# Kernel optimization log

Measured on AMD Instinct MI355X. Metric: run time of the kernel, lower is better.

## Reference

```python
import jax, jax.numpy as jnp
import numpy as np
import math

T, B, V, D = 8, 32, 50257, 256
N = 4096            # memory slots
H = 4               # attention heads
L = 2               # transformer layers
K = 3               # shift width
HALF = K // 2
WIN = 16            # controller window
RH, WH = 1, 1       # read / write heads
EPS = 1e-12


def _pe(win, d):
    pos = jnp.arange(win, dtype=jnp.float32)[:, None]
    div = jnp.exp(jnp.arange(0, d, 2, dtype=jnp.float32) * (-math.log(10000.0) / d))
    pe = jnp.zeros((win, d), dtype=jnp.float32)
    pe = pe.at[:, 0::2].set(jnp.sin(pos * div))
    pe = pe.at[:, 1::2].set(jnp.cos(pos * div))
    return pe[:, None, :]


def _ln(x, g, b, eps=1e-5):
    mu = x.mean(-1, keepdims=True)
    var = ((x - mu) ** 2).mean(-1, keepdims=True)
    return (x - mu) * jax.lax.rsqrt(var + eps) * g + b


def _mha(x, Wqkv, bqkv, Wo, bo):
    S, Bc, Dm = x.shape
    dh = Dm // H
    qkv = x @ Wqkv.T + bqkv
    q, k, v = jnp.split(qkv, 3, axis=-1)
    q = q.reshape(S, Bc, H, dh)
    k = k.reshape(S, Bc, H, dh)
    v = v.reshape(S, Bc, H, dh)
    logits = jnp.einsum('sbhd,tbhd->bhst', q, k) / math.sqrt(dh)
    a = jax.nn.softmax(logits, axis=-1)
    o = jnp.einsum('bhst,tbhd->sbhd', a, v).reshape(S, Bc, Dm)
    return o @ Wo.T + bo


def _addressing(key_v, beta, gate, shift, gamma, prev_w, memory):
    # key_v [B,M], beta/gate/gamma [B,1], shift [B,K], prev_w [B,N], memory [B,N,M]
    key_n = key_v / (jnp.linalg.norm(key_v, axis=-1, keepdims=True) + EPS)
    mem_n = memory / (jnp.linalg.norm(memory, axis=-1, keepdims=True) + EPS)
    cos = jnp.einsum('bnm,bm->bn', mem_n, key_n)
    wc = jax.nn.softmax(jax.nn.softplus(beta) * cos, axis=-1)
    g = jax.nn.sigmoid(gate)
    wg = g * wc + (1.0 - g) * prev_w
    s = jax.nn.softmax(shift, axis=-1)
    shifted = sum(s[:, k:k + 1] * jnp.roll(wg, k - HALF, axis=-1) for k in range(K))
    gp = 1.0 + jax.nn.softplus(gamma)
    wt = (shifted + EPS) ** gp
    return wt / (wt.sum(-1, keepdims=True) + EPS)


def setup_inputs() -> dict:
    key = jax.random.key(0)
    ks = iter(jax.random.split(key, 40))
    def w(shape, s=0.02):
        return jax.random.normal(next(ks), shape, jnp.float32) * s
    return {
        'tokens': jax.random.randint(next(ks), (T, B), 0, V, jnp.int32),
        'emb_W': w((V, D)),
        'read_gate_W': w((D, D)), 'read_gate_b': jnp.zeros((D,)),
        'film_W': w((2 * D, D)), 'film_b': jnp.zeros((2 * D,)),
        't_Wqkv': w((L, 3 * D, D)), 't_bqkv': jnp.zeros((L, 3 * D)),
        't_Wo': w((L, D, D)), 't_bo': jnp.zeros((L, D)),
        't_ln1_g': jnp.ones((L, D)), 't_ln1_b': jnp.zeros((L, D)),
        't_ln2_g': jnp.ones((L, D)), 't_ln2_b': jnp.zeros((L, D)),
        't_W1': w((L, 4 * D, D)), 't_b1': jnp.zeros((L, 4 * D)),
        't_W2': w((L, D, 4 * D)), 't_b2': jnp.zeros((L, D)),
        'out_ln_g': jnp.ones((D,)), 'out_ln_b': jnp.zeros((D,)),
        'lstm_Wih': w((2, 4 * D, D)), 'lstm_Whh': w((2, 4 * D, D)),
        'lstm_bih': jnp.zeros((2, 4 * D)), 'lstm_bhh': jnp.zeros((2, 4 * D)),
        'head_W': w((V, D)), 'head_b': jnp.zeros((V,)),
        'read_W': w((D + 3 + K, D)), 'read_b': jnp.zeros((D + 3 + K,)),
        'write_W': w((3 * D + 3 + K, D)), 'write_b': jnp.zeros((3 * D + 3 + K,)),
    }


def reference(tokens, emb_W, read_gate_W, read_gate_b, film_W, film_b,
              t_Wqkv, t_bqkv, t_Wo, t_bo, t_ln1_g, t_ln1_b, t_ln2_g, t_ln2_b,
              t_W1, t_b1, t_W2, t_b2, out_ln_g, out_ln_b,
              lstm_Wih, lstm_Whh, lstm_bih, lstm_bhh,
              head_W, head_b, read_W, read_b, write_W, write_b):
    pe = _pe(WIN, D)
    memory = jnp.zeros((B, N, D), jnp.float32)
    read_w = jnp.zeros((B, RH, N), jnp.float32).at[:, :, 0].set(1.0)
    write_w = jnp.zeros((B, WH, N), jnp.float32).at[:, :, 0].set(1.0)
    record = jnp.zeros((B, D), jnp.float32)
    hx = jnp.zeros((2, B, D), jnp.float32)
    cx = jnp.zeros((2, B, D), jnp.float32)
    hist = jnp.zeros((1, B, D), jnp.float32)
    logits_all = []
    for t in range(T):  # T fixed, sequential recurrence (context length grows)
        emb = emb_W[tokens[t]]                               # [B,D]
        r = jnp.einsum('bhn,bnm->bm', read_w, memory)        # sum over read heads
        fp = record @ film_W.T + film_b
        gam = 1.0 + jnp.tanh(fp[:, :D])
        bet = fp[:, D:]
        rg = jax.nn.sigmoid(record @ read_gate_W.T + read_gate_b)
        x_in = gam * emb + bet + rg * r
        ctx = jnp.concatenate([hist, x_in[None]], axis=0)
        if ctx.shape[0] > WIN:
            ctx = ctx[-WIN:]
        hist = ctx
        h = ctx + pe[:ctx.shape[0]]
        for l in range(L):  # norm_first pre-LN encoder layers (eval, relu FFN)
            h = h + _mha(_ln(h, t_ln1_g[l], t_ln1_b[l]), t_Wqkv[l], t_bqkv[l], t_Wo[l], t_bo[l])
            h = h + (jax.nn.relu(_ln(h, t_ln2_g[l], t_ln2_b[l]) @ t_W1[l].T + t_b1[l]) @ t_W2[l].T + t_b2[l])
        c_out = _ln(h[-1], out_ln_g, out_ln_b)
        # 2-layer LSTM single step (torch gate order i,f,g,o)
        x_l = c_out
        new_h, new_c = [], []
        for l in range(2):
            gates = x_l @ lstm_Wih[l].T + lstm_bih[l] + hx[l] @ lstm_Whh[l].T + lstm_bhh[l]
            i_g, f_g, g_g, o_g = jnp.split(gates, 4, axis=-1)
            c_new = jax.nn.sigmoid(f_g) * cx[l] + jax.nn.sigmoid(i_g) * jnp.tanh(g_g)
            h_new = jax.nn.sigmoid(o_g) * jnp.tanh(c_new)
            new_h.append(h_new); new_c.append(c_new)
            x_l = h_new
        hx = jnp.stack(new_h); cx = jnp.stack(new_c)
        record = hx[-1]
        c_out = c_out + x_l
        logits_all.append(c_out @ head_W.T + head_b)
        # read addressing
        rp = (c_out @ read_W.T + read_b).reshape(B, RH, -1)
        new_rw = []
        for hh in range(RH):
            p = rp[:, hh]
            new_rw.append(_addressing(p[:, :D], p[:, D:D + 1], p[:, D + 1:D + 2],
                                      p[:, D + 2:D + 2 + K], p[:, D + 2 + K:D + 3 + K],
                                      read_w[:, hh], memory))
        read_w = jnp.stack(new_rw, axis=1)
        # write addressing + erase/add (addressing uses pre-update memory)
        wp = (c_out @ write_W.T + write_b).reshape(B, WH, -1)
        mem_pre = memory
        new_ww = []
        for hh in range(WH):
            p = wp[:, hh]
            wt = _addressing(p[:, :D], p[:, D:D + 1], p[:, D + 1:D + 2],
                             p[:, D + 2:D + 2 + K], p[:, D + 2 + K:D + 3 + K],
                             write_w[:, hh], mem_pre)
            erase = jax.nn.sigmoid(p[:, D + 3 + K:2 * D + 3 + K])
            add = jnp.tanh(p[:, 2 * D + 3 + K:3 * D + 3 + K])
            memory = memory * (1.0 - wt[:, :, None] * erase[:, None, :]) + wt[:, :, None] * add[:, None, :]
            new_ww.append(wt)
        write_w = jnp.stack(new_ww, axis=1)
    return jnp.stack(logits_all, axis=0)  # [T, B, V]
```

## Files before the change

### kernel.cpp

```cpp
#include <hip/hip_runtime.h>
#include <math.h>

#define TT 8
#define BB 32
#define VV 50257
#define DD 256
#define NN 4096
#define EPS_ 1e-12f

typedef __attribute__((ext_vector_type(8))) short short8;
typedef __attribute__((ext_vector_type(4))) float f32x4;

__device__ __forceinline__ float sigf(float x) { return 1.f / (1.f + expf(-x)); }
__device__ __forceinline__ float softplusf_(float x) { return fmaxf(x, 0.f) + log1pf(expf(-fabsf(x))); }
__device__ __forceinline__ unsigned f2bf(float f) {
  union { float f; unsigned u; } c; c.f = f;
  return (c.u + 0x7FFFu + ((c.u >> 16) & 1u)) >> 16;
}
__device__ __forceinline__ float bf2f(unsigned u16) {
  union { unsigned u; float f; } c; c.u = u16 << 16; return c.f;
}

__device__ __forceinline__ float blk_sum(float v, float* s) {
#pragma unroll
  for (int o = 32; o > 0; o >>= 1) v += __shfl_down(v, o);
  __syncthreads();
  if ((threadIdx.x & 63) == 0) s[threadIdx.x >> 6] = v;
  __syncthreads();
  return s[0] + s[1] + s[2] + s[3];
}
__device__ __forceinline__ float blk_max(float v, float* s) {
#pragma unroll
  for (int o = 32; o > 0; o >>= 1) v = fmaxf(v, __shfl_down(v, o));
  __syncthreads();
  if ((threadIdx.x & 63) == 0) s[threadIdx.x >> 6] = v;
  __syncthreads();
  return fmaxf(fmaxf(s[0], s[1]), fmaxf(s[2], s[3]));
}

__global__ void init_k(float* rw, float* ww, float* hpe) {
  int i = blockIdx.x * 256 + threadIdx.x;
  if (i < BB) { rw[(size_t)i * NN] = 1.f; ww[(size_t)i * NN] = 1.f; }
  if (i < BB * DD) hpe[i] = (i & 1) ? 1.f : 0.f;
}

__global__ void cvtw_k(const float* __restrict__ W, unsigned short* __restrict__ Wh, int n4) {
  int i = blockIdx.x * 256 + threadIdx.x;
  if (i >= n4) return;
  float4 v = *(const float4*)(W + (size_t)i * 4);
  uint2 p;
  p.x = f2bf(v.x) | (f2bf(v.y) << 16);
  p.y = f2bf(v.z) | (f2bf(v.w) << 16);
  *(uint2*)(Wh + (size_t)i * 4) = p;
}

__global__ void catlstm_k(const float* __restrict__ Wih, const float* __restrict__ Whh,
                          const float* __restrict__ bih, const float* __restrict__ bhh,
                          unsigned short* __restrict__ Wc, float* __restrict__ cb) {
  int i = blockIdx.x * 256 + threadIdx.x;
  if (i >= 2 * 1024 * 512) return;
  int k = i & 511, np = (i >> 9) & 1023, l = i >> 19;
  int d = np >> 2, gate = np & 3;
  int src = gate * 256 + d;
  float v = (k < 256) ? Wih[((size_t)l * 1024 + src) * 256 + k]
                      : Whh[((size_t)l * 1024 + src) * 256 + (k - 256)];
  Wc[i] = (unsigned short)f2bf(v);
  if (k == 0) cb[l * 1024 + np] = bih[l * 1024 + src] + bhh[l * 1024 + src];
}

__global__ void catrw_k(const float* __restrict__ rW, const float* __restrict__ rb,
                        const float* __restrict__ wW, const float* __restrict__ wb,
                        unsigned short* __restrict__ Wrw, float* __restrict__ brw) {
  int i = blockIdx.x * 256 + threadIdx.x;
  if (i >= 1036 * 256) return;
  int k = i & 255, n = i >> 8;
  float v = (n < 262) ? rW[(size_t)n * 256 + k] : wW[(size_t)(n - 262) * 256 + k];
  Wrw[i] = (unsigned short)f2bf(v);
  if (k == 0) brw[n] = (n < 262) ? rb[n] : wb[n - 262];
}

__global__ void brc_k(const float* __restrict__ fb, const float* __restrict__ rb, float* __restrict__ brc) {
  int i = blockIdx.x * 256 + threadIdx.x;
  if (i < 512) brc[i] = fb[i];
  else if (i < 768) brc[i] = rb[i - 512];
}

__global__ __launch_bounds__(256) void ln0_k(const float* __restrict__ hpe,
                                             const float* __restrict__ g1, const float* __restrict__ b1,
                                             unsigned short* __restrict__ q1b) {
  __shared__ float s8[8];
  int b = blockIdx.x, d = threadIdx.x;
  float v = hpe[(size_t)b * 256 + d];
  float mu = blk_sum(v, s8) * (1.f / 256.f);
  float dd = v - mu;
  float var = blk_sum(dd * dd, s8) * (1.f / 256.f);
  float rs = rsqrtf(var + 1e-5f);
  q1b[(size_t)b * 256 + d] = (unsigned short)f2bf(dd * rs * g1[d] + b1[d]);
}

template <int EPI>
__global__ __launch_bounds__(256) void gA_k(const unsigned short* __restrict__ A,
                                            const unsigned short* __restrict__ W,
                                            const float* __restrict__ bias,
                                            float* __restrict__ Cf,
                                            unsigned short* __restrict__ Cb,
                                            int ldc, int Nlim) {
  const int tid = threadIdx.x, w = tid >> 6, l = tid & 63, r = l & 15, q = l >> 4;
  const int m0 = blockIdx.y * 32;
  const int n = blockIdx.x * 64 + w * 16 + r;
  const unsigned short* Ap = A + (size_t)m0 * 256;
  const unsigned short* Wp = W + (size_t)n * 256;
  f32x4 acc0 = {0.f, 0.f, 0.f, 0.f}, acc1 = {0.f, 0.f, 0.f, 0.f};
#pragma unroll
  for (int kt = 0; kt < 8; ++kt) {
    short8 a0 = *(const short8*)(Ap + r * 256 + kt * 32 + q * 8);
    short8 a1 = *(const short8*)(Ap + (16 + r) * 256 + kt * 32 + q * 8);
    short8 bf = *(const short8*)(Wp + kt * 32 + q * 8);
    acc0 = __builtin_amdgcn_mfma_f32_16x16x32_bf16(a0, bf, acc0, 0, 0, 0);
    acc1 = __builtin_amdgcn_mfma_f32_16x16x32_bf16(a1, bf, acc1, 0, 0, 0);
  }
  if (n >= Nlim) return;
  float bb = bias[n];
#pragma unroll
  for (int e = 0; e < 4; ++e) {
    int m1 = m0 + q * 4 + e, m2 = m1 + 16;
    float v1 = acc0[e] + bb, v2 = acc1[e] + bb;
    if constexpr (EPI == 0) {
      Cf[(size_t)m1 * ldc + n] = v1;
      Cf[(size_t)m2 * ldc + n] = v2;
    } else {
      Cb[(size_t)m1 * ldc + n] = (unsigned short)f2bf(fmaxf(v1, 0.f));
      Cb[(size_t)m2 * ldc + n] = (unsigned short)f2bf(fmaxf(v2, 0.f));
    }
  }
}

template <int K, int OLN>
__global__ __launch_bounds__(256) void gB_k(const unsigned short* __restrict__ A,
                                            const unsigned short* __restrict__ W,
                                            const float* __restrict__ bias,
                                            const float* __restrict__ resid,
                                            float* __restrict__ Hout,
                                            const float* __restrict__ lng,
                                            const float* __restrict__ lnb,
                                            unsigned short* __restrict__ Xb, int xstride,
                                            float* __restrict__ c_out) {
  __shared__ float hv[32][260];
  const int tid = threadIdx.x, w = tid >> 6, l = tid & 63, r = l & 15, q = l >> 4;
  const int m0 = blockIdx.x * 32;
  const unsigned short* Ap = A + (size_t)m0 * K;
  const unsigned short* Wp0 = W + (size_t)(w * 64 + 0 + r) * K;
  const unsigned short* Wp1 = W + (size_t)(w * 64 + 16 + r) * K;
  const unsigned short* Wp2 = W + (size_t)(w * 64 + 32 + r) * K;
  const unsigned short* Wp3 = W + (size_t)(w * 64 + 48 + r) * K;
  f32x4 acc0[4], acc1[4];
#pragma unroll
  for (int j = 0; j < 4; ++j) { acc0[j] = {0.f, 0.f, 0.f, 0.f}; acc1[j] = {0.f, 0.f, 0.f, 0.f}; }
#pragma unroll 4
  for (int kt = 0; kt < K / 32; ++kt) {
    short8 a0 = *(const short8*)(Ap + (size_t)r * K + kt * 32 + q * 8);
    short8 a1 = *(const short8*)(Ap + (size_t)(16 + r) * K + kt * 32 + q * 8);
    short8 b0 = *(const short8*)(Wp0 + kt * 32 + q * 8);
    short8 b1 = *(const short8*)(Wp1 + kt * 32 + q * 8);
    short8 b2 = *(const short8*)(Wp2 + kt * 32 + q * 8);
    short8 b3 = *(const short8*)(Wp3 + kt * 32 + q * 8);
    acc0[0] = __builtin_amdgcn_mfma_f32_16x16x32_bf16(a0, b0, acc0[0], 0, 0, 0);
    acc1[0] = __builtin_amdgcn_mfma_f32_16x16x32_bf16(a1, b0, acc1[0], 0, 0, 0);
    acc0[1] = __builtin_amdgcn_mfma_f32_16x16x32_bf16(a0, b1, acc0[1], 0, 0, 0);
    acc1[1] = __builtin_amdgcn_mfma_f32_16x16x32_bf16(a1, b1, acc1[1], 0, 0, 0);
    acc0[2] = __builtin_amdgcn_mfma_f32_16x16x32_bf16(a0, b2, acc0[2], 0, 0, 0);
    acc1[2] = __builtin_amdgcn_mfma_f32_16x16x32_bf16(a1, b2, acc1[2], 0, 0, 0);
    acc0[3] = __builtin_amdgcn_mfma_f32_16x16x32_bf16(a0, b3, acc0[3], 0, 0, 0);
    acc1[3] = __builtin_amdgcn_mfma_f32_16x16x32_bf16(a1, b3, acc1[3], 0, 0, 0);
  }
#pragma unroll
  for (int j = 0; j < 4; ++j) {
    int n = w * 64 + j * 16 + r;
    float bb = bias[n];
#pragma unroll
    for (int e = 0; e < 4; ++e) {
      int m1 = q * 4 + e, m2 = m1 + 16;
      float v1 = acc0[j][e] + bb + resid[(size_t)(m0 + m1) * 256 + n];
      float v2 = acc1[j][e] + bb + resid[(size_t)(m0 + m2) * 256 + n];
      Hout[(size_t)(m0 + m1) * 256 + n] = v1;
      Hout[(size_t)(m0 + m2) * 256 + n] = v2;
      hv[m1][n] = v1;
      hv[m2][n] = v2;
    }
  }
  __syncthreads();
  const float4 g4 = *(const float4*)(lng + l * 4);
  const float4 be4 = *(const float4*)(lnb + l * 4);
#pragma unroll
  for (int i = 0; i < 8; ++i) {
    int row = w * 8 + i;
    float4 v = *(const float4*)&hv[row][l * 4];
    float s1 = v.x + v.y + v.z + v.w;
    float s2 = v.x * v.x + v.y * v.y + v.z * v.z + v.w * v.w;
#pragma unroll
    for (int o = 32; o > 0; o >>= 1) { s1 += __shfl_xor(s1, o); s2 += __shfl_xor(s2, o); }
    float mu = s1 * (1.f / 256.f);
    float var = fmaxf(s2 * (1.f / 256.f) - mu * mu, 0.f);
    float rs = rsqrtf(var + 1e-5f);
    float y0 = (v.x - mu) * rs * g4.x + be4.x;
    float y1 = (v.y - mu) * rs * g4.y + be4.y;
    float y2 = (v.z - mu) * rs * g4.z + be4.z;
    float y3 = (v.w - mu) * rs * g4.w + be4.w;
    uint2 pk;
    pk.x = f2bf(y0) | (f2bf(y1) << 16);
    pk.y = f2bf(y2) | (f2bf(y3) << 16);
    *(uint2*)(Xb + (size_t)(m0 + row) * xstride + l * 4) = pk;
    if constexpr (OLN) {
      float4 cv = make_float4(y0, y1, y2, y3);
      *(float4*)(c_out + (size_t)(m0 + row) * 256 + l * 4) = cv;
    }
  }
}

template <int LAST>
__global__ __launch_bounds__(256) void gL_k(const unsigned short* __restrict__ A,
                                            const unsigned short* __restrict__ W,
                                            const float* __restrict__ cbias,
                                            float* __restrict__ cx,
                                            unsigned short* __restrict__ li_own,
                                            unsigned short* __restrict__ li_next,
                                            const float* __restrict__ c_outp,
                                            unsigned short* __restrict__ cfinb,
                                            unsigned short* __restrict__ record_b) {
  __shared__ float g[32][68];
  const int tid = threadIdx.x, w = tid >> 6, l = tid & 63, r = l & 15, q = l >> 4;
  const int n = blockIdx.x * 64 + w * 16 + r;
  const unsigned short* Wp = W + (size_t)n * 512;
  f32x4 acc0 = {0.f, 0.f, 0.f, 0.f}, acc1 = {0.f, 0.f, 0.f, 0.f};
#pragma unroll 4
  for (int kt = 0; kt < 16; ++kt) {
    short8 a0 = *(const short8*)(A + (size_t)r * 512 + kt * 32 + q * 8);
    short8 a1 = *(const short8*)(A + (size_t)(16 + r) * 512 + kt * 32 + q * 8);
    short8 bf = *(const short8*)(Wp + kt * 32 + q * 8);
    acc0 = __builtin_amdgcn_mfma_f32_16x16x32_bf16(a0, bf, acc0, 0, 0, 0);
    acc1 = __builtin_amdgcn_mfma_f32_16x16x32_bf16(a1, bf, acc1, 0, 0, 0);
  }
  float bb = cbias[n];
  int nb = w * 16 + r;
#pragma unroll
  for (int e = 0; e < 4; ++e) {
    g[q * 4 + e][nb] = acc0[e] + bb;
    g[16 + q * 4 + e][nb] = acc1[e] + bb;
  }
  __syncthreads();
#pragma unroll
  for (int h2 = 0; h2 < 2; ++h2) {
    int u = tid + 256 * h2;
    int b = u >> 4, dd = u & 15;
    int dg = blockIdx.x * 16 + dd;
    float gi = g[b][dd * 4 + 0], gf = g[b][dd * 4 + 1];
    float gg = g[b][dd * 4 + 2], go = g[b][dd * 4 + 3];
    float c = sigf(gf) * cx[b * 256 + dg] + sigf(gi) * tanhf(gg);
    float hN = sigf(go) * tanhf(c);
    cx[b * 256 + dg] = c;
    li_own[(size_t)b * 512 + 256 + dg] = (unsigned short)f2bf(hN);
    if constexpr (LAST) {
      record_b[b * 256 + dg] = (unsigned short)f2bf(hN);
      cfinb[b * 256 + dg] = (unsigned short)f2bf(c_outp[b * 256 + dg] + hN);
    } else {
      li_next[(size_t)b * 512 + dg] = (unsigned short)f2bf(hN);
    }
  }
}

__global__ __launch_bounds__(256) void xinpw_k(const int* __restrict__ tokens,
                                               const float* __restrict__ embW,
                                               const float* __restrict__ fp,
                                               const float* __restrict__ rvec,
                                               const float* __restrict__ g1, const float* __restrict__ b1,
                                               float* __restrict__ hpe,
                                               unsigned short* __restrict__ q1b, int t) {
  __shared__ float s8[8];
  int b = blockIdx.x, d = threadIdx.x;
  float gam = 1.f + tanhf(fp[(size_t)b * 768 + d]);
  float bet = fp[(size_t)b * 768 + 256 + d];
  float rg = sigf(fp[(size_t)b * 768 + 512 + d]);
  int tok = tokens[t * BB + b];
  float emb = embW[(size_t)tok * 256 + d];
  float ang = (float)(t + 1) * expf(-logf(10000.f) * (float)(d & ~1) / 256.f);
  float pe = (d & 1) ? cosf(ang) : sinf(ang);
  float x = gam * emb + bet + rg * rvec[b * 256 + d] + pe;
  hpe[((size_t)(t + 1) * BB + b) * 256 + d] = x;
  float mu = blk_sum(x, s8) * (1.f / 256.f);
  float dd = x - mu;
  float var = blk_sum(dd * dd, s8) * (1.f / 256.f);
  float rs = rsqrtf(var + 1e-5f);
  q1b[((size_t)(t + 1) * BB + b) * 256 + d] = (unsigned short)f2bf(dd * rs * g1[d] + b1[d]);
}

__global__ __launch_bounds__(128) void attn_k(const float* __restrict__ qkv,
                                              unsigned short* __restrict__ ao, int S) {
  int bh = blockIdx.x;
  int b = bh >> 2, h = bh & 3;
  __shared__ float q[9][64], k[9][64], v[9][64], lg[9][12];
  int tid = threadIdx.x;
  for (int i = tid; i < S * 64; i += 128) {
    int s = i >> 6, d = i & 63;
    const float* base = qkv + (size_t)(s * BB + b) * 768 + h * 64 + d;
    q[s][d] = base[0]; k[s][d] = base[256]; v[s][d] = base[512];
  }
  __syncthreads();
  for (int p = tid; p < S * S; p += 128) {
    int s = p / S, t2 = p % S;
    float acc = 0.f;
    for (int d = 0; d < 64; ++d) acc += q[s][d] * k[t2][d];
    lg[s][t2] = acc * 0.125f;
  }
  __syncthreads();
  if (tid < S) {
    float mx = -1e30f;
    for (int t2 = 0; t2 < S; ++t2) mx = fmaxf(mx, lg[tid][t2]);
    float sum = 0.f;
    for (int t2 = 0; t2 < S; ++t2) { float e = expf(lg[tid][t2] - mx); lg[tid][t2] = e; sum += e; }
    float inv = 1.f / sum;
    for (int t2 = 0; t2 < S; ++t2) lg[tid][t2] *= inv;
  }
  __syncthreads();
  for (int i = tid; i < S * 64; i += 128) {
    int s = i >> 6, d = i & 63;
    float o = 0.f;
    for (int t2 = 0; t2 < S; ++t2) o += lg[s][t2] * v[t2][d];
    ao[(size_t)(s * BB + b) * 256 + h * 64 + d] = (unsigned short)f2bf(o);
  }
}

__global__ __launch_bounds__(64) void attnl_k(const float* __restrict__ qkv,
                                              unsigned short* __restrict__ ao, int S) {
  int bh = blockIdx.x;
  int b = bh >> 2, h = bh & 3;
  int d = threadIdx.x;
  __shared__ float sc[9];
  float qd = qkv[(size_t)((S - 1) * BB + b) * 768 + h * 64 + d];
  for (int j = 0; j < S; ++j) {
    float p = qd * qkv[(size_t)(j * BB + b) * 768 + h * 64 + 256 + d];
#pragma unroll
    for (int o = 32; o > 0; o >>= 1) p += __shfl_down(p, o);
    if (d == 0) sc[j] = p * 0.125f;
  }
  __syncthreads();
  float mx = -1e30f;
  for (int j = 0; j < S; ++j) mx = fmaxf(mx, sc[j]);
  float pj[9], sum = 0.f;
  for (int j = 0; j < S; ++j) { pj[j] = expf(sc[j] - mx); sum += pj[j]; }
  float inv = 1.f / sum;
  float o = 0.f;
  for (int j = 0; j < S; ++j) o += pj[j] * inv * qkv[(size_t)(j * BB + b) * 768 + h * 64 + 512 + d];
  ao[(size_t)b * 256 + h * 64 + d] = (unsigned short)f2bf(o);
}

__global__ __launch_bounds__(256) void head_k(const unsigned short* __restrict__ Wh,
                                              const unsigned short* __restrict__ Ah,
                                              const float* __restrict__ hb,
                                              float* __restrict__ out) {
  const int tid = threadIdx.x;
  const int w = tid >> 6, l = tid & 63;
  const int r = l & 15, q = l >> 4;
  const int n = blockIdx.x * 64 + w * 16 + r;
  const int nc = n < VV ? n : VV - 1;
  const short* Ap = (const short*)Ah;
  const short* Wp = (const short*)Wh + (size_t)nc * 256;
  short8 a0[8], a1[8], bf[8];
#pragma unroll
  for (int kt = 0; kt < 8; ++kt) {
    a0[kt] = *(const short8*)(Ap + r * 256 + kt * 32 + q * 8);
    a1[kt] = *(const short8*)(Ap + (16 + r) * 256 + kt * 32 + q * 8);
    bf[kt] = *(const short8*)(Wp + kt * 32 + q * 8);
  }
  f32x4 acc0 = {0.f, 0.f, 0.f, 0.f}, acc1 = {0.f, 0.f, 0.f, 0.f};
#pragma unroll
  for (int kt = 0; kt < 8; ++kt) {
    acc0 = __builtin_amdgcn_mfma_f32_16x16x32_bf16(a0[kt], bf[kt], acc0, 0, 0, 0);
    acc1 = __builtin_amdgcn_mfma_f32_16x16x32_bf16(a1[kt], bf[kt], acc1, 0, 0, 0);
  }
  if (n < VV) {
    float bb = hb[n];
#pragma unroll
    for (int e = 0; e < 4; ++e) {
      int m = q * 4 + e;
      out[(size_t)m * VV + n] = acc0[e] + bb;
      out[(size_t)(16 + m) * VV + n] = acc1[e] + bb;
    }
  }
}

__global__ __launch_bounds__(256) void passA_k(const unsigned short* __restrict__ mem,
                                               const float* __restrict__ rpwp,
                                               float* __restrict__ dr,
                                               float* __restrict__ dw,
                                               float* __restrict__ nrm) {
  __shared__ float kr[256], kw[256];
  int b = blockIdx.y, tid = threadIdx.x;
  kr[tid] = rpwp[(size_t)b * 1036 + tid];
  kw[tid] = rpwp[(size_t)b * 1036 + 262 + tid];
  __syncthreads();
  int w = tid >> 6, lane = tid & 63;
  float4 kr4 = *(float4*)&kr[lane * 4];
  float4 kw4 = *(float4*)&kw[lane * 4];
  int n0 = blockIdx.x * 16 + w * 4;
  for (int rr = 0; rr < 4; ++rr) {
    int n = n0 + rr;
    const unsigned short* row = mem + ((size_t)b * NN + n) * 256;
    uint2 p = *(const uint2*)(row + lane * 4);
    float m0 = bf2f(p.x & 0xffffu), m1 = bf2f(p.x >> 16);
    float m2 = bf2f(p.y & 0xffffu), m3 = bf2f(p.y >> 16);
    float pr = m0 * kr4.x + m1 * kr4.y + m2 * kr4.z + m3 * kr4.w;
    float pw = m0 * kw4.x + m1 * kw4.y + m2 * kw4.z + m3 * kw4.w;
    float pn = m0 * m0 + m1 * m1 + m2 * m2 + m3 * m3;
#pragma unroll
    for (int o = 32; o > 0; o >>= 1) {
      pr += __shfl_down(pr, o); pw += __shfl_down(pw, o); pn += __shfl_down(pn, o);
    }
    if (lane == 0) {
      dr[(size_t)b * NN + n] = pr;
      dw[(size_t)b * NN + n] = pw;
      nrm[(size_t)b * NN + n] = pn;
    }
  }
}

__global__ __launch_bounds__(256) void addr_k(const float* __restrict__ dr,
                                              const float* __restrict__ dw,
                                              const float* __restrict__ nrm,
                                              const float* __restrict__ rpwp,
                                              float* rw, float* ww,
                                              float* __restrict__ ea,
                                              float* __restrict__ rvec) {
  __shared__ float wg[4096];
  __shared__ float s8[8];
  int head = blockIdx.x & 1, b = blockIdx.x >> 1;
  int tid = threadIdx.x;
  const float* p = rpwp + (size_t)b * 1036 + (head ? 262 : 0);
  const float* dot = (head ? dw : dr) + (size_t)b * NN;
  const float* n2 = nrm + (size_t)b * NN;
  float* wout = (head ? ww : rw) + (size_t)b * NN;

  float kv = p[tid];
  float kn = sqrtf(blk_sum(kv * kv, s8)) + EPS_;
  float beta = p[256], gate = p[257], sh0 = p[258], sh1 = p[259], sh2 = p[260], gamma = p[261];
  float spb = softplusf_(beta);
  float g = sigf(gate);
  float mx3 = fmaxf(sh0, fmaxf(sh1, sh2));
  float e0 = expf(sh0 - mx3), e1 = expf(sh1 - mx3), e2 = expf(sh2 - mx3);
  float esum = e0 + e1 + e2;
  float s0 = e0 / esum, s1 = e1 / esum, s2 = e2 / esum;
  float gp = 1.f + softplusf_(gamma);

  float l[16];
  float lmax = -1e30f;
#pragma unroll
  for (int i = 0; i < 16; ++i) {
    int n = tid + i * 256;
    float cs = dot[n] / ((sqrtf(n2[n]) + EPS_) * kn);
    l[i] = spb * cs;
    lmax = fmaxf(lmax, l[i]);
  }
  float Mx = blk_max(lmax, s8);
  float es = 0.f;
#pragma unroll
  for (int i = 0; i < 16; ++i) { l[i] = expf(l[i] - Mx); es += l[i]; }
  float SS = blk_sum(es, s8);
  float inv = 1.f / SS;
#pragma unroll
  for (int i = 0; i < 16; ++i) {
    int n = tid + i * 256;
    wg[n] = g * l[i] * inv + (1.f - g) * wout[n];
  }
  __syncthreads();
  float wt[16];
  float wsum = 0.f;
#pragma unroll
  for (int i = 0; i < 16; ++i) {
    int n = tid + i * 256;
    float sh = s0 * wg[(n + 1) & 4095] + s1 * wg[n] + s2 * wg[(n + 4095) & 4095];
    wt[i] = powf(sh + EPS_, gp);
    wsum += wt[i];
  }
  float WS = blk_sum(wsum, s8) + EPS_;
  float winv = 1.f / WS;
#pragma unroll
  for (int i = 0; i < 16; ++i) wout[tid + i * 256] = wt[i] * winv;

  if (head) {
    ea[(size_t)b * 512 + tid] = sigf(p[262 + tid]);
    ea[(size_t)b * 512 + 256 + tid] = tanhf(p[518 + tid]);
  } else {
    rvec[(size_t)b * 256 + tid] = 0.f;
  }
}

template <int FIRST>
__global__ __launch_bounds__(256) void passB_k(unsigned short* mem, const float* __restrict__ ww,
                                               const float* __restrict__ rw,
                                               const float* __restrict__ ea,
                                               float* __restrict__ rvec) {
  __shared__ float eS[256], aS[256];
  __shared__ float rred[4][256];
  int b = blockIdx.y, tid = threadIdx.x;
  eS[tid] = ea[(size_t)b * 512 + tid];
  aS[tid] = ea[(size_t)b * 512 + 256 + tid];
  __syncthreads();
  int w = tid >> 6, lane = tid & 63;
  float4 e4 = *(float4*)&eS[lane * 4];
  float4 a4 = *(float4*)&aS[lane * 4];
  float4 racc = make_float4(0.f, 0.f, 0.f, 0.f);
  int n0 = blockIdx.x * 128 + w * 32;
  for (int rr = 0; rr < 32; ++rr) {
    int n = n0 + rr;
    float wt = ww[(size_t)b * NN + n];
    float rwv = rw[(size_t)b * NN + n];
    unsigned short* row = mem + ((size_t)b * NN + n) * 256;
    float m0, m1, m2, m3;
    if (FIRST) {
      m0 = wt * a4.x; m1 = wt * a4.y; m2 = wt * a4.z; m3 = wt * a4.w;
    } else {
      uint2 p = *(const uint2*)(row + lane * 4);
      m0 = bf2f(p.x & 0xffffu) * (1.f - wt * e4.x) + wt * a4.x;
      m1 = bf2f(p.x >> 16) * (1.f - wt * e4.y) + wt * a4.y;
      m2 = bf2f(p.y & 0xffffu) * (1.f - wt * e4.z) + wt * a4.z;
      m3 = bf2f(p.y >> 16) * (1.f - wt * e4.w) + wt * a4.w;
    }
    uint2 pk;
    pk.x = f2bf(m0) | (f2bf(m1) << 16);
    pk.y = f2bf(m2) | (f2bf(m3) << 16);
    *(uint2*)(row + lane * 4) = pk;
    racc.x += rwv * m0; racc.y += rwv * m1; racc.z += rwv * m2; racc.w += rwv * m3;
  }
  rred[w][lane * 4 + 0] = racc.x;
  rred[w][lane * 4 + 1] = racc.y;
  rred[w][lane * 4 + 2] = racc.z;
  rred[w][lane * 4 + 3] = racc.w;
  __syncthreads();
  float s = rred[0][tid] + rred[1][tid] + rred[2][tid] + rred[3][tid];
  atomicAdd(rvec + (size_t)b * 256 + tid, s);
}

extern "C" void kernel_launch(void* const* d_in, const int* in_sizes, int n_in,
                              void* d_out, int out_size, void* d_ws, size_t ws_size,
                              hipStream_t stream) {
  const int* tokens = (const int*)d_in[0];
  const float* emb_W = (const float*)d_in[1];
  const float* read_gate_W = (const float*)d_in[2];
  const float* read_gate_b = (const float*)d_in[3];
  const float* film_W = (const float*)d_in[4];
  const float* film_b = (const float*)d_in[5];
  const float* t_Wqkv = (const float*)d_in[6];
  const float* t_bqkv = (const float*)d_in[7];
  const float* t_Wo = (const float*)d_in[8];
  const float* t_bo = (const float*)d_in[9];
  const float* t_ln1_g = (const float*)d_in[10];
  const float* t_ln1_b = (const float*)d_in[11];
  const float* t_ln2_g = (const float*)d_in[12];
  const float* t_ln2_b = (const float*)d_in[13];
  const float* t_W1 = (const float*)d_in[14];
  const float* t_b1 = (const float*)d_in[15];
  const float* t_W2 = (const float*)d_in[16];
  const float* t_b2 = (const float*)d_in[17];
  const float* out_ln_g = (const float*)d_in[18];
  const float* out_ln_b = (const float*)d_in[19];
  const float* lstm_Wih = (const float*)d_in[20];
  const float* lstm_Whh = (const float*)d_in[21];
  const float* lstm_bih = (const float*)d_in[22];
  const float* lstm_bhh = (const float*)d_in[23];
  const float* head_W = (const float*)d_in[24];
  const float* head_b = (const float*)d_in[25];
  const float* read_W = (const float*)d_in[26];
  const float* read_b = (const float*)d_in[27];
  const float* write_W = (const float*)d_in[28];
  const float* write_b = (const float*)d_in[29];
  float* out = (float*)d_out;

  float* ws = (float*)d_ws;
  size_t off = 0;
  float* read_w = ws + off; off += (size_t)BB * NN;
  float* write_w = ws + off; off += (size_t)BB * NN;
  float* cx = ws + off; off += 2 * BB * DD;
  float* r_vec = ws + off; off += BB * DD;
  float* dot_r = ws + off; off += (size_t)BB * NN;
  float* dot_w = ws + off; off += (size_t)BB * NN;
  float* norm2 = ws + off; off += (size_t)BB * NN;
  unsigned short* record_b = (unsigned short*)(ws + off); off += BB * DD / 2;
  unsigned short* lstm_in_b = (unsigned short*)(ws + off); off += 2 * BB * 512 / 2;
  size_t zero_floats = off;
  unsigned short* memory = (unsigned short*)(ws + off); off += (size_t)BB * NN * DD / 2;
  float* hpe = ws + off; off += 9 * BB * DD;
  float* h = ws + off; off += 9 * BB * DD;
  float* h2 = ws + off; off += BB * DD;
  float* qkvC = ws + off; off += 9 * BB * 768;
  float* qkv2 = ws + off; off += 9 * BB * 768;
  float* fp = ws + off; off += BB * 768;
  float* c_out = ws + off; off += BB * DD;
  float* rpwp = ws + off; off += BB * 1036;
  float* ea = ws + off; off += BB * 2 * DD;
  unsigned short* q1b = (unsigned short*)(ws + off); off += 9 * BB * DD / 2;
  unsigned short* q2b = (unsigned short*)(ws + off); off += 9 * BB * DD / 2;
  unsigned short* x2b = (unsigned short*)(ws + off); off += 9 * BB * DD / 2;
  unsigned short* x2b2 = (unsigned short*)(ws + off); off += BB * DD / 2;
  unsigned short* ao_b = (unsigned short*)(ws + off); off += 9 * BB * DD / 2;
  unsigned short* ao2_b = (unsigned short*)(ws + off); off += BB * DD / 2;
  unsigned short* mid_b = (unsigned short*)(ws + off); off += 9 * BB * 1024 / 2;
  unsigned short* cfinb = (unsigned short*)(ws + off); off += BB * DD / 2;
  unsigned short* Wh = (unsigned short*)(ws + off); off += (size_t)VV * 256 / 2;
  unsigned short* Wq_b = (unsigned short*)(ws + off); off += 2 * 768 * 256 / 2;
  unsigned short* Wo_b = (unsigned short*)(ws + off); off += 2 * 256 * 256 / 2;
  unsigned short* W1_b = (unsigned short*)(ws + off); off += 2 * 1024 * 256 / 2;
  unsigned short* W2_b = (unsigned short*)(ws + off); off += 2 * 256 * 1024 / 2;
  unsigned short* Wc_b = (unsigned short*)(ws + off); off += 2 * 1024 * 512 / 2;
  unsigned short* Wrw_b = (unsigned short*)(ws + off); off += 1088 * 256 / 2;
  unsigned short* FR_b = (unsigned short*)(ws + off); off += 768 * 256 / 2;
  float* cb2 = ws + off; off += 2 * 1024;
  float* brw = ws + off; off += 1040;
  float* brc = ws + off; off += 768;
  if (ws_size < off * sizeof(float)) return;

  (void)hipMemsetAsync(ws, 0, zero_floats * sizeof(float), stream);
  (void)hipMemsetAsync(Wrw_b + (size_t)1036 * 256, 0, (size_t)52 * 256 * 2, stream);
  init_k<<<32, 256, 0, stream>>>(read_w, write_w, hpe);
  cvtw_k<<<(VV * 256 / 4 + 255) / 256, 256, 0, stream>>>(head_W, Wh, VV * 256 / 4);
  cvtw_k<<<(2 * 768 * 256 / 4 + 255) / 256, 256, 0, stream>>>(t_Wqkv, Wq_b, 2 * 768 * 256 / 4);
  cvtw_k<<<(2 * 256 * 256 / 4 + 255) / 256, 256, 0, stream>>>(t_Wo, Wo_b, 2 * 256 * 256 / 4);
  cvtw_k<<<(2 * 1024 * 256 / 4 + 255) / 256, 256, 0, stream>>>(t_W1, W1_b, 2 * 1024 * 256 / 4);
  cvtw_k<<<(2 * 256 * 1024 / 4 + 255) / 256, 256, 0, stream>>>(t_W2, W2_b, 2 * 256 * 1024 / 4);
  cvtw_k<<<(512 * 256 / 4 + 255) / 256, 256, 0, stream>>>(film_W, FR_b, 512 * 256 / 4);
  cvtw_k<<<(256 * 256 / 4 + 255) / 256, 256, 0, stream>>>(read_gate_W, FR_b + 512 * 256, 256 * 256 / 4);
  catlstm_k<<<4096, 256, 0, stream>>>(lstm_Wih, lstm_Whh, lstm_bih, lstm_bhh, Wc_b, cb2);
  catrw_k<<<1036, 256, 0, stream>>>(read_W, read_b, write_W, write_b, Wrw_b, brw);
  brc_k<<<3, 256, 0, stream>>>(film_b, read_gate_b, brc);
  ln0_k<<<BB, 256, 0, stream>>>(hpe, t_ln1_g, t_ln1_b, q1b);
  gA_k<0><<<dim3(12, 1), 256, 0, stream>>>(q1b, Wq_b, t_bqkv, qkvC, nullptr, 768, 768);

  for (int t = 0; t < TT; ++t) {
    const int S = t + 2;

    gA_k<0><<<dim3(12, 1), 256, 0, stream>>>(record_b, FR_b, brc, fp, nullptr, 768, 768);
    xinpw_k<<<BB, 256, 0, stream>>>(tokens, emb_W, fp, r_vec, t_ln1_g, t_ln1_b, hpe, q1b, t);
    gA_k<0><<<dim3(12, 1), 256, 0, stream>>>(q1b + (size_t)(t + 1) * BB * 256, Wq_b, t_bqkv,
                                             qkvC + (size_t)(t + 1) * BB * 768, nullptr, 768, 768);
    attn_k<<<BB * 4, 128, 0, stream>>>(qkvC, ao_b, S);
    gB_k<256, 0><<<S, 256, 0, stream>>>(ao_b, Wo_b, t_bo, hpe, h, t_ln2_g, t_ln2_b, x2b, 256, nullptr);
    gA_k<1><<<dim3(16, S), 256, 0, stream>>>(x2b, W1_b, t_b1, nullptr, mid_b, 1024, 1024);
    gB_k<1024, 0><<<S, 256, 0, stream>>>(mid_b, W2_b, t_b2, h, h, t_ln1_g + 256, t_ln1_b + 256, q2b, 256, nullptr);

    gA_k<0><<<dim3(12, S), 256, 0, stream>>>(q2b, Wq_b + 768 * 256, t_bqkv + 768, qkv2, nullptr, 768, 768);
    attnl_k<<<BB * 4, 64, 0, stream>>>(qkv2, ao2_b, S);
    gB_k<256, 0><<<1, 256, 0, stream>>>(ao2_b, Wo_b + 256 * 256, t_bo + 256, h + (size_t)(S - 1) * BB * 256,
                                        h2, t_ln2_g + 256, t_ln2_b + 256, x2b2, 256, nullptr);
    gA_k<1><<<dim3(16, 1), 256, 0, stream>>>(x2b2, W1_b + 1024 * 256, t_b1 + 1024, nullptr, mid_b, 1024, 1024);
    gB_k<1024, 1><<<1, 256, 0, stream>>>(mid_b, W2_b + 256 * 1024, t_b2 + 256, h2, h2,
                                         out_ln_g, out_ln_b, lstm_in_b, 512, c_out);

    gL_k<0><<<16, 256, 0, stream>>>(lstm_in_b, Wc_b, cb2, cx, lstm_in_b, lstm_in_b + BB * 512,
                                    nullptr, nullptr, nullptr);
    gL_k<1><<<16, 256, 0, stream>>>(lstm_in_b + BB * 512, Wc_b + (size_t)1024 * 512, cb2 + 1024,
                                    cx + BB * DD, lstm_in_b + BB * 512, nullptr, c_out, cfinb, record_b);

    head_k<<<(VV + 63) / 64, 256, 0, stream>>>(Wh, cfinb, head_b, out + (size_t)t * BB * VV);

    if (t < TT - 1) {
      gA_k<0><<<dim3(17, 1), 256, 0, stream>>>(cfinb, Wrw_b, brw, rpwp, nullptr, 1036, 1036);
      if (t > 0)
        passA_k<<<dim3(NN / 16, BB), 256, 0, stream>>>(memory, rpwp, dot_r, dot_w, norm2);
      addr_k<<<2 * BB, 256, 0, stream>>>(dot_r, dot_w, norm2, rpwp, read_w, write_w, ea, r_vec);
      if (t == 0)
        passB_k<1><<<dim3(NN / 128, BB), 256, 0, stream>>>(memory, write_w, read_w, ea, r_vec);
      else
        passB_k<0><<<dim3(NN / 128, BB), 256, 0, stream>>>(memory, write_w, read_w, ea, r_vec);
    }
  }
}
```

Before: 1.679 ms.

## Fuse transformer tail into one kernel and merge head GEMM with memory pass

Each layer's Wo projection, LN2, FFN (W1 with ReLU, then W2) and the following LayerNorm now run in a single tail_k kernel, with the FFN intermediate kept in shared memory in 256-wide chunks instead of round-tripping through global memory. The vocabulary head GEMM is merged with the memory dot-product pass into one launch (fusePA_k), and the read/write projection and FiLM projection GEMMs are combined into auxg_k. This cuts kernel launches and intermediate global traffic on the serial per-timestep path. The cost is that the FFN runs on only S blocks (or one block for layer 2), so parallelism is low, and the head GEMM now sits on the dependency path right before addressing.

```diff
diff --git a/kernel.cpp b/kernel.cpp
--- a/kernel.cpp
+++ b/kernel.cpp
@@ -98,99 +98,57 @@
   q1b[(size_t)b * 256 + d] = (unsigned short)f2bf(dd * rs * g1[d] + b1[d]);
 }
 
-template <int EPI>
+__device__ __forceinline__ void gA32f_dev(const unsigned short* __restrict__ A,
+                                          const unsigned short* __restrict__ W,
+                                          const float* __restrict__ bias,
+                                          float* __restrict__ Cf, int ldc, int Nlim, int nblk) {
+  const int tid = threadIdx.x, w = tid >> 6, l = tid & 63, r = l & 15, q = l >> 4;
+  const int n = nblk * 64 + w * 16 + r;
+  const unsigned short* Wp = W + (size_t)n * 256;
+  f32x4 acc0 = {0.f, 0.f, 0.f, 0.f}, acc1 = {0.f, 0.f, 0.f, 0.f};
+#pragma unroll
+  for (int kt = 0; kt < 8; ++kt) {
+    short8 a0 = *(const short8*)(A + r * 256 + kt * 32 + q * 8);
+    short8 a1 = *(const short8*)(A + (16 + r) * 256 + kt * 32 + q * 8);
+    short8 bf = *(const short8*)(Wp + kt * 32 + q * 8);
+    acc0 = __builtin_amdgcn_mfma_f32_16x16x32_bf16(a0, bf, acc0, 0, 0, 0);
+    acc1 = __builtin_amdgcn_mfma_f32_16x16x32_bf16(a1, bf, acc1, 0, 0, 0);
+  }
+  if (n >= Nlim) return;
+  float bb = bias[n];
+#pragma unroll
+  for (int e = 0; e < 4; ++e) {
+    int m1 = q * 4 + e, m2 = m1 + 16;
+    Cf[(size_t)m1 * ldc + n] = acc0[e] + bb;
+    Cf[(size_t)m2 * ldc + n] = acc1[e] + bb;
+  }
+}
+
 __global__ __launch_bounds__(256) void gA_k(const unsigned short* __restrict__ A,
                                             const unsigned short* __restrict__ W,
                                             const float* __restrict__ bias,
-                                            float* __restrict__ Cf,
-                                            unsigned short* __restrict__ Cb,
-                                            int ldc, int Nlim) {
-  const int tid = threadIdx.x, w = tid >> 6, l = tid & 63, r = l & 15, q = l >> 4;
-  const int m0 = blockIdx.y * 32;
-  const int n = blockIdx.x * 64 + w * 16 + r;
-  const unsigned short* Ap = A + (size_t)m0 * 256;
-  const unsigned short* Wp = W + (size_t)n * 256;
-  f32x4 acc0 = {0.f, 0.f, 0.f, 0.f}, acc1 = {0.f, 0.f, 0.f, 0.f};
-#pragma unroll
-  for (int kt = 0; kt < 8; ++kt) {
-    short8 a0 = *(const short8*)(Ap + r * 256 + kt * 32 + q * 8);
-    short8 a1 = *(const short8*)(Ap + (16 + r) * 256 + kt * 32 + q * 8);
-    short8 bf = *(const short8*)(Wp + kt * 32 + q * 8);
-    acc0 = __builtin_amdgcn_mfma_f32_16x16x32_bf16(a0, bf, acc0, 0, 0, 0);
-    acc1 = __builtin_amdgcn_mfma_f32_16x16x32_bf16(a1, bf, acc1, 0, 0, 0);
-  }
-  if (n >= Nlim) return;
-  float bb = bias[n];
-#pragma unroll
-  for (int e = 0; e < 4; ++e) {
-    int m1 = m0 + q * 4 + e, m2 = m1 + 16;
-    float v1 = acc0[e] + bb, v2 = acc1[e] + bb;
-    if constexpr (EPI == 0) {
-      Cf[(size_t)m1 * ldc + n] = v1;
-      Cf[(size_t)m2 * ldc + n] = v2;
-    } else {
-      Cb[(size_t)m1 * ldc + n] = (unsigned short)f2bf(fmaxf(v1, 0.f));
-      Cb[(size_t)m2 * ldc + n] = (unsigned short)f2bf(fmaxf(v2, 0.f));
-    }
-  }
-}
-
-template <int K, int OLN>
-__global__ __launch_bounds__(256) void gB_k(const unsigned short* __restrict__ A,
-                                            const unsigned short* __restrict__ W,
-                                            const float* __restrict__ bias,
-                                            const float* __restrict__ resid,
-                                            float* __restrict__ Hout,
-                                            const float* __restrict__ lng,
-                                            const float* __restrict__ lnb,
-                                            unsigned short* __restrict__ Xb, int xstride,
-                                            float* __restrict__ c_out) {
-  __shared__ float hv[32][260];
-  const int tid = threadIdx.x, w = tid >> 6, l = tid & 63, r = l & 15, q = l >> 4;
-  const int m0 = blockIdx.x * 32;
-  const unsigned short* Ap = A + (size_t)m0 * K;
-  const unsigned short* Wp0 = W + (size_t)(w * 64 + 0 + r) * K;
-  const unsigned short* Wp1 = W + (size_t)(w * 64 + 16 + r) * K;
-  const unsigned short* Wp2 = W + (size_t)(w * 64 + 32 + r) * K;
-  const unsigned short* Wp3 = W + (size_t)(w * 64 + 48 + r) * K;
-  f32x4 acc0[4], acc1[4];
-#pragma unroll
-  for (int j = 0; j < 4; ++j) { acc0[j] = {0.f, 0.f, 0.f, 0.f}; acc1[j] = {0.f, 0.f, 0.f, 0.f}; }
-#pragma unroll 4
-  for (int kt = 0; kt < K / 32; ++kt) {
-    short8 a0 = *(const short8*)(Ap + (size_t)r * K + kt * 32 + q * 8);
-    short8 a1 = *(const short8*)(Ap + (size_t)(16 + r) * K + kt * 32 + q * 8);
-    short8 b0 = *(const short8*)(Wp0 + kt * 32 + q * 8);
-    short8 b1 = *(const short8*)(Wp1 + kt * 32 + q * 8);
-    short8 b2 = *(const short8*)(Wp2 + kt * 32 + q * 8);
-    short8 b3 = *(const short8*)(Wp3 + kt * 32 + q * 8);
-    acc0[0] = __builtin_amdgcn_mfma_f32_16x16x32_bf16(a0, b0, acc0[0], 0, 0, 0);
-    acc1[0] = __builtin_amdgcn_mfma_f32_16x16x32_bf16(a1, b0, acc1[0], 0, 0, 0);
-    acc0[1] = __builtin_amdgcn_mfma_f32_16x16x32_bf16(a0, b1, acc0[1], 0, 0, 0);
-    acc1[1] = __builtin_amdgcn_mfma_f32_16x16x32_bf16(a1, b1, acc1[1], 0, 0, 0);
-    acc0[2] = __builtin_amdgcn_mfma_f32_16x16x32_bf16(a0, b2, acc0[2], 0, 0, 0);
-    acc1[2] = __builtin_amdgcn_mfma_f32_16x16x32_bf16(a1, b2, acc1[2], 0, 0, 0);
-    acc0[3] = __builtin_amdgcn_mfma_f32_16x16x32_bf16(a0, b3, acc0[3], 0, 0, 0);
-    acc1[3] = __builtin_amdgcn_mfma_f32_16x16x32_bf16(a1, b3, acc1[3], 0, 0, 0);
-  }
-#pragma unroll
-  for (int j = 0; j < 4; ++j) {
-    int n = w * 64 + j * 16 + r;
-    float bb = bias[n];
-#pragma unroll
-    for (int e = 0; e < 4; ++e) {
-      int m1 = q * 4 + e, m2 = m1 + 16;
-      float v1 = acc0[j][e] + bb + resid[(size_t)(m0 + m1) * 256 + n];
-      float v2 = acc1[j][e] + bb + resid[(size_t)(m0 + m2) * 256 + n];
-      Hout[(size_t)(m0 + m1) * 256 + n] = v1;
-      Hout[(size_t)(m0 + m2) * 256 + n] = v2;
-      hv[m1][n] = v1;
-      hv[m2][n] = v2;
-    }
-  }
-  __syncthreads();
-  const float4 g4 = *(const float4*)(lng + l * 4);
-  const float4 be4 = *(const float4*)(lnb + l * 4);
+                                            float* __restrict__ Cf, int ldc, int Nlim) {
+  gA32f_dev(A + (size_t)blockIdx.y * 32 * 256, W, bias,
+            Cf + (size_t)blockIdx.y * 32 * ldc, ldc, Nlim, blockIdx.x);
+}
+
+__global__ __launch_bounds__(256) void auxg_k(const unsigned short* __restrict__ cfinb,
+                                              const unsigned short* __restrict__ Wrw,
+                                              const float* __restrict__ brw, float* __restrict__ rpwp,
+                                              const unsigned short* __restrict__ record_b,
+                                              const unsigned short* __restrict__ FRw,
+                                              const float* __restrict__ brc, float* __restrict__ fp) {
+  if (blockIdx.x < 17) gA32f_dev(cfinb, Wrw, brw, rpwp, 1036, 1036, blockIdx.x);
+  else gA32f_dev(record_b, FRw, brc, fp, 768, 768, blockIdx.x - 17);
+}
+
+__device__ __forceinline__ void ln_rows(float (*hv)[260], const float* __restrict__ g,
+                                        const float* __restrict__ be,
+                                        unsigned short* __restrict__ out, int ostride,
+                                        float* __restrict__ fout) {
+  const int tid = threadIdx.x, w = tid >> 6, l = tid & 63;
+  const float4 g4 = *(const float4*)(g + l * 4);
+  const float4 b4 = *(const float4*)(be + l * 4);
 #pragma unroll
   for (int i = 0; i < 8; ++i) {
     int row = w * 8 + i;
@@ -202,19 +160,235 @@
     float mu = s1 * (1.f / 256.f);
     float var = fmaxf(s2 * (1.f / 256.f) - mu * mu, 0.f);
     float rs = rsqrtf(var + 1e-5f);
-    float y0 = (v.x - mu) * rs * g4.x + be4.x;
-    float y1 = (v.y - mu) * rs * g4.y + be4.y;
-    float y2 = (v.z - mu) * rs * g4.z + be4.z;
-    float y3 = (v.w - mu) * rs * g4.w + be4.w;
+    float y0 = (v.x - mu) * rs * g4.x + b4.x;
+    float y1 = (v.y - mu) * rs * g4.y + b4.y;
+    float y2 = (v.z - mu) * rs * g4.z + b4.z;
+    float y3 = (v.w - mu) * rs * g4.w + b4.w;
     uint2 pk;
     pk.x = f2bf(y0) | (f2bf(y1) << 16);
     pk.y = f2bf(y2) | (f2bf(y3) << 16);
-    *(uint2*)(Xb + (size_t)(m0 + row) * xstride + l * 4) = pk;
-    if constexpr (OLN) {
+    *(uint2*)(out + (size_t)row * ostride + l * 4) = pk;
+    if (fout) {
       float4 cv = make_float4(y0, y1, y2, y3);
-      *(float4*)(c_out + (size_t)(m0 + row) * 256 + l * 4) = cv;
-    }
-  }
+      *(float4*)(fout + (size_t)row * 256 + l * 4) = cv;
+    }
+  }
+}
+
+template <int FIN>
+__global__ __launch_bounds__(256, 1) void tail_k(
+    const unsigned short* __restrict__ Asrc, const unsigned short* __restrict__ Wo,
+    const float* __restrict__ bo, const float* __restrict__ resid,
+    const float* __restrict__ ln2g, const float* __restrict__ ln2b,
+    const unsigned short* __restrict__ W1, const float* __restrict__ b1,
+    const unsigned short* __restrict__ W2, const float* __restrict__ b2,
+    float* __restrict__ Hout,
+    const float* __restrict__ lnFg, const float* __restrict__ lnFb,
+    unsigned short* __restrict__ Xout, int xstride, float* __restrict__ c_out) {
+  __shared__ float bufA[32][260];
+  __shared__ unsigned short x2s[32][264];
+  unsigned short (*midc)[264] = (unsigned short(*)[264])&bufA[0][0];
+
+  const int tid = threadIdx.x, w = tid >> 6, l = tid & 63, r = l & 15, q = l >> 4;
+  const int m0 = blockIdx.x * 32;
+  const unsigned short* Ap = Asrc + (size_t)m0 * 256;
+  const float* residp = resid + (size_t)m0 * 256;
+
+  float vres0[4][4], vres1[4][4];
+
+  {
+    const unsigned short* Wp0 = Wo + (size_t)(w * 64 + 0 + r) * 256;
+    const unsigned short* Wp1 = Wo + (size_t)(w * 64 + 16 + r) * 256;
+    const unsigned short* Wp2 = Wo + (size_t)(w * 64 + 32 + r) * 256;
+    const unsigned short* Wp3 = Wo + (size_t)(w * 64 + 48 + r) * 256;
+    f32x4 acc0[4], acc1[4];
+#pragma unroll
+    for (int j = 0; j < 4; ++j) { acc0[j] = {0.f, 0.f, 0.f, 0.f}; acc1[j] = {0.f, 0.f, 0.f, 0.f}; }
+#pragma unroll
+    for (int kt = 0; kt < 8; ++kt) {
+      short8 a0 = *(const short8*)(Ap + r * 256 + kt * 32 + q * 8);
+      short8 a1 = *(const short8*)(Ap + (16 + r) * 256 + kt * 32 + q * 8);
+      short8 b0v = *(const short8*)(Wp0 + kt * 32 + q * 8);
+      short8 b1v = *(const short8*)(Wp1 + kt * 32 + q * 8);
+      short8 b2v = *(const short8*)(Wp2 + kt * 32 + q * 8);
+      short8 b3v = *(const short8*)(Wp3 + kt * 32 + q * 8);
+      acc0[0] = __builtin_amdgcn_mfma_f32_16x16x32_bf16(a0, b0v, acc0[0], 0, 0, 0);
+      acc1[0] = __builtin_amdgcn_mfma_f32_16x16x32_bf16(a1, b0v, acc1[0], 0, 0, 0);
+      acc0[1] = __builtin_amdgcn_mfma_f32_16x16x32_bf16(a0, b1v, acc0[1], 0, 0, 0);
+      acc1[1] = __builtin_amdgcn_mfma_f32_16x16x32_bf16(a1, b1v, acc1[1], 0, 0, 0);
+      acc0[2] = __builtin_amdgcn_mfma_f32_16x16x32_bf16(a0, b2v, acc0[2], 0, 0, 0);
+      acc1[2] = __builtin_amdgcn_mfma_f32_16x16x32_bf16(a1, b2v, acc1[2], 0, 0, 0);
+      acc0[3] = __builtin_amdgcn_mfma_f32_16x16x32_bf16(a0, b3v, acc0[3], 0, 0, 0);
+      acc1[3] = __builtin_amdgcn_mfma_f32_16x16x32_bf16(a1, b3v, acc1[3], 0, 0, 0);
+    }
+#pragma unroll
+    for (int j = 0; j < 4; ++j) {
+      int n = w * 64 + j * 16 + r;
+      float bb = bo[n];
+#pragma unroll
+      for (int e = 0; e < 4; ++e) {
+        int m1 = q * 4 + e, m2 = m1 + 16;
+        float v1 = acc0[j][e] + bb + residp[(size_t)m1 * 256 + n];
+        float v2 = acc1[j][e] + bb + residp[(size_t)m2 * 256 + n];
+        vres0[j][e] = v1; vres1[j][e] = v2;
+        bufA[m1][n] = v1; bufA[m2][n] = v2;
+      }
+    }
+  }
+  __syncthreads();
+  ln_rows(bufA, ln2g, ln2b, &x2s[0][0], 264, nullptr);
+  __syncthreads();
+  short8 fa0[8], fa1[8];
+#pragma unroll
+  for (int kt = 0; kt < 8; ++kt) {
+    fa0[kt] = *(const short8*)&x2s[r][kt * 32 + q * 8];
+    fa1[kt] = *(const short8*)&x2s[16 + r][kt * 32 + q * 8];
+  }
+  f32x4 cac0[4], cac1[4];
+#pragma unroll
+  for (int j = 0; j < 4; ++j) { cac0[j] = {0.f, 0.f, 0.f, 0.f}; cac1[j] = {0.f, 0.f, 0.f, 0.f}; }
+
+  for (int c = 0; c < 4; ++c) {
+    {
+      const unsigned short* Q0 = W1 + (size_t)(c * 256 + w * 64 + 0 + r) * 256;
+      const unsigned short* Q1 = W1 + (size_t)(c * 256 + w * 64 + 16 + r) * 256;
+      const unsigned short* Q2 = W1 + (size_t)(c * 256 + w * 64 + 32 + r) * 256;
+      const unsigned short* Q3 = W1 + (size_t)(c * 256 + w * 64 + 48 + r) * 256;
+      f32x4 ba0[4], ba1[4];
+#pragma unroll
+      for (int j = 0; j < 4; ++j) { ba0[j] = {0.f, 0.f, 0.f, 0.f}; ba1[j] = {0.f, 0.f, 0.f, 0.f}; }
+#pragma unroll
+      for (int kt = 0; kt < 8; ++kt) {
+        short8 b0v = *(const short8*)(Q0 + kt * 32 + q * 8);
+        short8 b1v = *(const short8*)(Q1 + kt * 32 + q * 8);
+        short8 b2v = *(const short8*)(Q2 + kt * 32 + q * 8);
+        short8 b3v = *(const short8*)(Q3 + kt * 32 + q * 8);
+        ba0[0] = __builtin_amdgcn_mfma_f32_16x16x32_bf16(fa0[kt], b0v, ba0[0], 0, 0, 0);
+        ba1[0] = __builtin_amdgcn_mfma_f32_16x16x32_bf16(fa1[kt], b0v, ba1[0], 0, 0, 0);
+        ba0[1] = __builtin_amdgcn_mfma_f32_16x16x32_bf16(fa0[kt], b1v, ba0[1], 0, 0, 0);
+        ba1[1] = __builtin_amdgcn_mfma_f32_16x16x32_bf16(fa1[kt], b1v, ba1[1], 0, 0, 0);
+        ba0[2] = __builtin_amdgcn_mfma_f32_16x16x32_bf16(fa0[kt], b2v, ba0[2], 0, 0, 0);
+        ba1[2] = __builtin_amdgcn_mfma_f32_16x16x32_bf16(fa1[kt], b2v, ba1[2], 0, 0, 0);
+        ba0[3] = __builtin_amdgcn_mfma_f32_16x16x32_bf16(fa0[kt], b3v, ba0[3], 0, 0, 0);
+        ba1[3] = __builtin_amdgcn_mfma_f32_16x16x32_bf16(fa1[kt], b3v, ba1[3], 0, 0, 0);
+      }
+#pragma unroll
+      for (int j = 0; j < 4; ++j) {
+        int nl = w * 64 + j * 16 + r;
+        float bb = b1[c * 256 + nl];
+#pragma unroll
+        for (int e = 0; e < 4; ++e) {
+          int m1 = q * 4 + e, m2 = m1 + 16;
+          midc[m1][nl] = (unsigned short)f2bf(fmaxf(ba0[j][e] + bb, 0.f));
+          midc[m2][nl] = (unsigned short)f2bf(fmaxf(ba1[j][e] + bb, 0.f));
+        }
+      }
+    }
+    __syncthreads();
+    {
+      const unsigned short* P0 = W2 + (size_t)(w * 64 + 0 + r) * 1024 + c * 256;
+      const unsigned short* P1 = W2 + (size_t)(w * 64 + 16 + r) * 1024 + c * 256;
+      const unsigned short* P2 = W2 + (size_t)(w * 64 + 32 + r) * 1024 + c * 256;
+      const unsigned short* P3 = W2 + (size_t)(w * 64 + 48 + r) * 1024 + c * 256;
+#pragma unroll
+      for (int kt = 0; kt < 8; ++kt) {
+        short8 a0 = *(const short8*)&midc[r][kt * 32 + q * 8];
+        short8 a1 = *(const short8*)&midc[16 + r][kt * 32 + q * 8];
+        short8 b0v = *(const short8*)(P0 + kt * 32 + q * 8);
+        short8 b1v = *(const short8*)(P1 + kt * 32 + q * 8);
+        short8 b2v = *(const short8*)(P2 + kt * 32 + q * 8);
+        short8 b3v = *(const short8*)(P3 + kt * 32 + q * 8);
+        cac0[0] = __builtin_amdgcn_mfma_f32_16x16x32_bf16(a0, b0v, cac0[0], 0, 0, 0);
+        cac1[0] = __builtin_amdgcn_mfma_f32_16x16x32_bf16(a1, b0v, cac1[0], 0, 0, 0);
+        cac0[1] = __builtin_amdgcn_mfma_f32_16x16x32_bf16(a0, b1v, cac0[1], 0, 0, 0);
+        cac1[1] = __builtin_amdgcn_mfma_f32_16x16x32_bf16(a1, b1v, cac1[1], 0, 0, 0);
+        cac0[2] = __builtin_amdgcn_mfma_f32_16x16x32_bf16(a0, b2v, cac0[2], 0, 0, 0);
+        cac1[2] = __builtin_amdgcn_mfma_f32_16x16x32_bf16(a1, b2v, cac1[2], 0, 0, 0);
+        cac0[3] = __builtin_amdgcn_mfma_f32_16x16x32_bf16(a0, b3v, cac0[3], 0, 0, 0);
+        cac1[3] = __builtin_amdgcn_mfma_f32_16x16x32_bf16(a1, b3v, cac1[3], 0, 0, 0);
+      }
+    }
+    __syncthreads();
+  }
+#pragma unroll
+  for (int j = 0; j < 4; ++j) {
+    int n = w * 64 + j * 16 + r;
+    float bb = b2[n];
+#pragma unroll
+    for (int e = 0; e < 4; ++e) {
+      int m1 = q * 4 + e, m2 = m1 + 16;
+      float fv1 = cac0[j][e] + bb + vres0[j][e];
+      float fv2 = cac1[j][e] + bb + vres1[j][e];
+      if constexpr (FIN == 0) {
+        Hout[(size_t)(m0 + m1) * 256 + n] = fv1;
+        Hout[(size_t)(m0 + m2) * 256 + n] = fv2;
+      }
+      bufA[m1][n] = fv1;
+      bufA[m2][n] = fv2;
+    }
+  }
+  __syncthreads();
+  ln_rows(bufA, lnFg, lnFb, Xout + (size_t)m0 * xstride, xstride, FIN ? c_out : nullptr);
+}
+
+__global__ __launch_bounds__(128) void attn_k(const float* __restrict__ qkv,
+                                              unsigned short* __restrict__ ao, int S) {
+  int bh = blockIdx.x;
+  int b = bh >> 2, h = bh & 3;
+  __shared__ float q[9][64], k[9][64], v[9][64], lg[9][12];
+  int tid = threadIdx.x;
+  for (int i = tid; i < S * 64; i += 128) {
+    int s = i >> 6, d = i & 63;
+    const float* base = qkv + (size_t)(s * BB + b) * 768 + h * 64 + d;
+    q[s][d] = base[0]; k[s][d] = base[256]; v[s][d] = base[512];
+  }
+  __syncthreads();
+  for (int p = tid; p < S * S; p += 128) {
+    int s = p / S, t2 = p % S;
+    float acc = 0.f;
+    for (int d = 0; d < 64; ++d) acc += q[s][d] * k[t2][d];
+    lg[s][t2] = acc * 0.125f;
+  }
+  __syncthreads();
+  if (tid < S) {
+    float mx = -1e30f;
+    for (int t2 = 0; t2 < S; ++t2) mx = fmaxf(mx, lg[tid][t2]);
+    float sum = 0.f;
+    for (int t2 = 0; t2 < S; ++t2) { float e = expf(lg[tid][t2] - mx); lg[tid][t2] = e; sum += e; }
+    float inv = 1.f / sum;
+    for (int t2 = 0; t2 < S; ++t2) lg[tid][t2] *= inv;
+  }
+  __syncthreads();
+  for (int i = tid; i < S * 64; i += 128) {
+    int s = i >> 6, d = i & 63;
+    float o = 0.f;
+    for (int t2 = 0; t2 < S; ++t2) o += lg[s][t2] * v[t2][d];
+    ao[(size_t)(s * BB + b) * 256 + h * 64 + d] = (unsigned short)f2bf(o);
+  }
+}
+
+__global__ __launch_bounds__(64) void attnl_k(const float* __restrict__ qkv,
+                                              unsigned short* __restrict__ ao, int S) {
+  int bh = blockIdx.x;
+  int b = bh >> 2, h = bh & 3;
+  int d = threadIdx.x;
+  __shared__ float sc[9];
+  float qd = qkv[(size_t)((S - 1) * BB + b) * 768 + h * 64 + d];
+  for (int j = 0; j < S; ++j) {
+    float p = qd * qkv[(size_t)(j * BB + b) * 768 + h * 64 + 256 + d];
+#pragma unroll
+    for (int o = 32; o > 0; o >>= 1) p += __shfl_down(p, o);
+    if (d == 0) sc[j] = p * 0.125f;
+  }
+  __syncthreads();
+  float mx = -1e30f;
+  for (int j = 0; j < S; ++j) mx = fmaxf(mx, sc[j]);
+  float pj[9], sum = 0.f;
+  for (int j = 0; j < S; ++j) { pj[j] = expf(sc[j] - mx); sum += pj[j]; }
+  float inv = 1.f / sum;
+  float o = 0.f;
+  for (int j = 0; j < S; ++j) o += pj[j] * inv * qkv[(size_t)(j * BB + b) * 768 + h * 64 + 512 + d];
+  ao[(size_t)b * 256 + h * 64 + d] = (unsigned short)f2bf(o);
 }
 
 template <int LAST>
@@ -293,121 +467,64 @@
   q1b[((size_t)(t + 1) * BB + b) * 256 + d] = (unsigned short)f2bf(dd * rs * g1[d] + b1[d]);
 }
 
-__global__ __launch_bounds__(128) void attn_k(const float* __restrict__ qkv,
-                                              unsigned short* __restrict__ ao, int S) {
-  int bh = blockIdx.x;
-  int b = bh >> 2, h = bh & 3;
-  __shared__ float q[9][64], k[9][64], v[9][64], lg[9][12];
-  int tid = threadIdx.x;
-  for (int i = tid; i < S * 64; i += 128) {
-    int s = i >> 6, d = i & 63;
-    const float* base = qkv + (size_t)(s * BB + b) * 768 + h * 64 + d;
-    q[s][d] = base[0]; k[s][d] = base[256]; v[s][d] = base[512];
-  }
-  __syncthreads();
-  for (int p = tid; p < S * S; p += 128) {
-    int s = p / S, t2 = p % S;
-    float acc = 0.f;
-    for (int d = 0; d < 64; ++d) acc += q[s][d] * k[t2][d];
-    lg[s][t2] = acc * 0.125f;
-  }
-  __syncthreads();
-  if (tid < S) {
-    float mx = -1e30f;
-    for (int t2 = 0; t2 < S; ++t2) mx = fmaxf(mx, lg[tid][t2]);
-    float sum = 0.f;
-    for (int t2 = 0; t2 < S; ++t2) { float e = expf(lg[tid][t2] - mx); lg[tid][t2] = e; sum += e; }
-    float inv = 1.f / sum;
-    for (int t2 = 0; t2 < S; ++t2) lg[tid][t2] *= inv;
-  }
-  __syncthreads();
-  for (int i = tid; i < S * 64; i += 128) {
-    int s = i >> 6, d = i & 63;
-    float o = 0.f;
-    for (int t2 = 0; t2 < S; ++t2) o += lg[s][t2] * v[t2][d];
-    ao[(size_t)(s * BB + b) * 256 + h * 64 + d] = (unsigned short)f2bf(o);
-  }
-}
-
-__global__ __launch_bounds__(64) void attnl_k(const float* __restrict__ qkv,
-                                              unsigned short* __restrict__ ao, int S) {
-  int bh = blockIdx.x;
-  int b = bh >> 2, h = bh & 3;
-  int d = threadIdx.x;
-  __shared__ float sc[9];
-  float qd = qkv[(size_t)((S - 1) * BB + b) * 768 + h * 64 + d];
-  for (int j = 0; j < S; ++j) {
-    float p = qd * qkv[(size_t)(j * BB + b) * 768 + h * 64 + 256 + d];
-#pragma unroll
-    for (int o = 32; o > 0; o >>= 1) p += __shfl_down(p, o);
-    if (d == 0) sc[j] = p * 0.125f;
-  }
-  __syncthreads();
-  float mx = -1e30f;
-  for (int j = 0; j < S; ++j) mx = fmaxf(mx, sc[j]);
-  float pj[9], sum = 0.f;
-  for (int j = 0; j < S; ++j) { pj[j] = expf(sc[j] - mx); sum += pj[j]; }
-  float inv = 1.f / sum;
-  float o = 0.f;
-  for (int j = 0; j < S; ++j) o += pj[j] * inv * qkv[(size_t)(j * BB + b) * 768 + h * 64 + 512 + d];
-  ao[(size_t)b * 256 + h * 64 + d] = (unsigned short)f2bf(o);
-}
-
-__global__ __launch_bounds__(256) void head_k(const unsigned short* __restrict__ Wh,
-                                              const unsigned short* __restrict__ Ah,
-                                              const float* __restrict__ hb,
-                                              float* __restrict__ out) {
+__global__ __launch_bounds__(256) void fusePA_k(const unsigned short* __restrict__ Wh,
+                                                const unsigned short* __restrict__ Ah,
+                                                const float* __restrict__ hb,
+                                                float* __restrict__ out,
+                                                const unsigned short* __restrict__ mem,
+                                                const float* __restrict__ rpwp,
+                                                float* __restrict__ dr,
+                                                float* __restrict__ dw,
+                                                float* __restrict__ nrm) {
+  __shared__ float kr[256], kw[256];
+  const int bid = blockIdx.x;
   const int tid = threadIdx.x;
-  const int w = tid >> 6, l = tid & 63;
-  const int r = l & 15, q = l >> 4;
-  const int n = blockIdx.x * 64 + w * 16 + r;
-  const int nc = n < VV ? n : VV - 1;
-  const short* Ap = (const short*)Ah;
-  const short* Wp = (const short*)Wh + (size_t)nc * 256;
-  short8 a0[8], a1[8], bf[8];
-#pragma unroll
-  for (int kt = 0; kt < 8; ++kt) {
-    a0[kt] = *(const short8*)(Ap + r * 256 + kt * 32 + q * 8);
-    a1[kt] = *(const short8*)(Ap + (16 + r) * 256 + kt * 32 + q * 8);
-    bf[kt] = *(const short8*)(Wp + kt * 32 + q * 8);
-  }
-  f32x4 acc0 = {0.f, 0.f, 0.f, 0.f}, acc1 = {0.f, 0.f, 0.f, 0.f};
-#pragma unroll
-  for (int kt = 0; kt < 8; ++kt) {
-    acc0 = __builtin_amdgcn_mfma_f32_16x16x32_bf16(a0[kt], bf[kt], acc0, 0, 0, 0);
-    acc1 = __builtin_amdgcn_mfma_f32_16x16x32_bf16(a1[kt], bf[kt], acc1, 0, 0, 0);
-  }
-  if (n < VV) {
-    float bb = hb[n];
-#pragma unroll
-    for (int e = 0; e < 4; ++e) {
-      int m = q * 4 + e;
-      out[(size_t)m * VV + n] = acc0[e] + bb;
-      out[(size_t)(16 + m) * VV + n] = acc1[e] + bb;
-    }
-  }
-}
-
-__global__ __launch_bounds__(256) void passA_k(const unsigned short* __restrict__ mem,
-                                               const float* __restrict__ rpwp,
-                                               float* __restrict__ dr,
-                                               float* __restrict__ dw,
-                                               float* __restrict__ nrm) {
-  __shared__ float kr[256], kw[256];
-  int b = blockIdx.y, tid = threadIdx.x;
-  kr[tid] = rpwp[(size_t)b * 1036 + tid];
-  kw[tid] = rpwp[(size_t)b * 1036 + 262 + tid];
+  if (bid < 786) {
+    const int w = tid >> 6, l = tid & 63;
+    const int r = l & 15, q = l >> 4;
+    const int n = bid * 64 + w * 16 + r;
+    const int nc = n < VV ? n : VV - 1;
+    const short* Ap = (const short*)Ah;
+    const short* Wp = (const short*)Wh + (size_t)nc * 256;
+    short8 a0[8], a1[8], bf[8];
+#pragma unroll
+    for (int kt = 0; kt < 8; ++kt) {
+      a0[kt] = *(const short8*)(Ap + r * 256 + kt * 32 + q * 8);
+      a1[kt] = *(const short8*)(Ap + (16 + r) * 256 + kt * 32 + q * 8);
+      bf[kt] = *(const short8*)(Wp + kt * 32 + q * 8);
+    }
+    f32x4 acc0 = {0.f, 0.f, 0.f, 0.f}, acc1 = {0.f, 0.f, 0.f, 0.f};
+#pragma unroll
+    for (int kt = 0; kt < 8; ++kt) {
+      acc0 = __builtin_amdgcn_mfma_f32_16x16x32_bf16(a0[kt], bf[kt], acc0, 0, 0, 0);
+      acc1 = __builtin_amdgcn_mfma_f32_16x16x32_bf16(a1[kt], bf[kt], acc1, 0, 0, 0);
+    }
+    if (n < VV) {
+      float bb = hb[n];
+#pragma unroll
+      for (int e = 0; e < 4; ++e) {
+        int m = q * 4 + e;
+        out[(size_t)m * VV + n] = acc0[e] + bb;
+        out[(size_t)(16 + m) * VV + n] = acc1[e] + bb;
+      }
+    }
+    return;
+  }
+  const int idx = bid - 786;
+  const int bx = idx & 255, by = idx >> 8;
+  kr[tid] = rpwp[(size_t)by * 1036 + tid];
+  kw[tid] = rpwp[(size_t)by * 1036 + 262 + tid];
   __syncthreads();
   int w = tid >> 6, lane = tid & 63;
   float4 kr4 = *(float4*)&kr[lane * 4];
   float4 kw4 = *(float4*)&kw[lane * 4];
-  int n0 = blockIdx.x * 16 + w * 4;
+  int n0 = bx * 16 + w * 4;
   for (int rr = 0; rr < 4; ++rr) {
     int n = n0 + rr;
-    const unsigned short* row = mem + ((size_t)b * NN + n) * 256;
-    uint2 p = *(const uint2*)(row + lane * 4);
-    float m0 = bf2f(p.x & 0xffffu), m1 = bf2f(p.x >> 16);
-    float m2 = bf2f(p.y & 0xffffu), m3 = bf2f(p.y >> 16);
+    const unsigned short* row = mem + ((size_t)by * NN + n) * 256;
+    uint2 pck = *(const uint2*)(row + lane * 4);
+    float m0 = bf2f(pck.x & 0xffffu), m1 = bf2f(pck.x >> 16);
+    float m2 = bf2f(pck.y & 0xffffu), m3 = bf2f(pck.y >> 16);
     float pr = m0 * kr4.x + m1 * kr4.y + m2 * kr4.z + m3 * kr4.w;
     float pw = m0 * kw4.x + m1 * kw4.y + m2 * kw4.z + m3 * kw4.w;
     float pn = m0 * m0 + m1 * m1 + m2 * m2 + m3 * m3;
@@ -416,9 +533,9 @@
       pr += __shfl_down(pr, o); pw += __shfl_down(pw, o); pn += __shfl_down(pn, o);
     }
     if (lane == 0) {
-      dr[(size_t)b * NN + n] = pr;
-      dw[(size_t)b * NN + n] = pw;
-      nrm[(size_t)b * NN + n] = pn;
+      dr[(size_t)by * NN + n] = pr;
+      dw[(size_t)by * NN + n] = pw;
+      nrm[(size_t)by * NN + n] = pn;
     }
   }
 }
@@ -589,7 +706,6 @@
   unsigned short* memory = (unsigned short*)(ws + off); off += (size_t)BB * NN * DD / 2;
   float* hpe = ws + off; off += 9 * BB * DD;
   float* h = ws + off; off += 9 * BB * DD;
-  float* h2 = ws + off; off += BB * DD;
   float* qkvC = ws + off; off += 9 * BB * 768;
   float* qkv2 = ws + off; off += 9 * BB * 768;
   float* fp = ws + off; off += BB * 768;
@@ -598,11 +714,8 @@
   float* ea = ws + off; off += BB * 2 * DD;
   unsigned short* q1b = (unsigned short*)(ws + off); off += 9 * BB * DD / 2;
   unsigned short* q2b = (unsigned short*)(ws + off); off += 9 * BB * DD / 2;
-  unsigned short* x2b = (unsigned short*)(ws + off); off += 9 * BB * DD / 2;
-  unsigned short* x2b2 = (unsigned short*)(ws + off); off += BB * DD / 2;
-  unsigned short* ao_b = (unsigned short*)(ws + off); off += 9 * BB * DD / 2;
+  unsigned short* ao1_b = (unsigned short*)(ws + off); off += 9 * BB * DD / 2;
   unsigned short* ao2_b = (unsigned short*)(ws + off); off += BB * DD / 2;
-  unsigned short* mid_b = (unsigned short*)(ws + off); off += 9 * BB * 1024 / 2;
   unsigned short* cfinb = (unsigned short*)(ws + off); off += BB * DD / 2;
   unsigned short* Wh = (unsigned short*)(ws + off); off += (size_t)VV * 256 / 2;
   unsigned short* Wq_b = (unsigned short*)(ws + off); off += 2 * 768 * 256 / 2;
@@ -631,44 +744,47 @@
   catrw_k<<<1036, 256, 0, stream>>>(read_W, read_b, write_W, write_b, Wrw_b, brw);
   brc_k<<<3, 256, 0, stream>>>(film_b, read_gate_b, brc);
   ln0_k<<<BB, 256, 0, stream>>>(hpe, t_ln1_g, t_ln1_b, q1b);
-  gA_k<0><<<dim3(12, 1), 256, 0, stream>>>(q1b, Wq_b, t_bqkv, qkvC, nullptr, 768, 768);
+  gA_k<<<dim3(12, 1), 256, 0, stream>>>(q1b, Wq_b, t_bqkv, qkvC, 768, 768);
+  gA_k<<<dim3(12, 1), 256, 0, stream>>>(record_b, FR_b, brc, fp, 768, 768);
 
   for (int t = 0; t < TT; ++t) {
     const int S = t + 2;
 
-    gA_k<0><<<dim3(12, 1), 256, 0, stream>>>(record_b, FR_b, brc, fp, nullptr, 768, 768);
     xinpw_k<<<BB, 256, 0, stream>>>(tokens, emb_W, fp, r_vec, t_ln1_g, t_ln1_b, hpe, q1b, t);
-    gA_k<0><<<dim3(12, 1), 256, 0, stream>>>(q1b + (size_t)(t + 1) * BB * 256, Wq_b, t_bqkv,
-                                             qkvC + (size_t)(t + 1) * BB * 768, nullptr, 768, 768);
-    attn_k<<<BB * 4, 128, 0, stream>>>(qkvC, ao_b, S);
-    gB_k<256, 0><<<S, 256, 0, stream>>>(ao_b, Wo_b, t_bo, hpe, h, t_ln2_g, t_ln2_b, x2b, 256, nullptr);
-    gA_k<1><<<dim3(16, S), 256, 0, stream>>>(x2b, W1_b, t_b1, nullptr, mid_b, 1024, 1024);
-    gB_k<1024, 0><<<S, 256, 0, stream>>>(mid_b, W2_b, t_b2, h, h, t_ln1_g + 256, t_ln1_b + 256, q2b, 256, nullptr);
-
-    gA_k<0><<<dim3(12, S), 256, 0, stream>>>(q2b, Wq_b + 768 * 256, t_bqkv + 768, qkv2, nullptr, 768, 768);
+    gA_k<<<dim3(12, 1), 256, 0, stream>>>(q1b + (size_t)(t + 1) * BB * 256, Wq_b, t_bqkv,
+                                          qkvC + (size_t)(t + 1) * BB * 768, 768, 768);
+    attn_k<<<BB * 4, 128, 0, stream>>>(qkvC, ao1_b, S);
+    tail_k<0><<<S, 256, 0, stream>>>(ao1_b, Wo_b, t_bo, hpe, t_ln2_g, t_ln2_b,
+                                     W1_b, t_b1, W2_b, t_b2, h,
+                                     t_ln1_g + 256, t_ln1_b + 256, q2b, 256, nullptr);
+    gA_k<<<dim3(12, S), 256, 0, stream>>>(q2b, Wq_b + 768 * 256, t_bqkv + 768, qkv2, 768, 768);
     attnl_k<<<BB * 4, 64, 0, stream>>>(qkv2, ao2_b, S);
-    gB_k<256, 0><<<1, 256, 0, stream>>>(ao2_b, Wo_b + 256 * 256, t_bo + 256, h + (size_t)(S - 1) * BB * 256,
-                                        h2, t_ln2_g + 256, t_ln2_b + 256, x2b2, 256, nullptr);
-    gA_k<1><<<dim3(16, 1), 256, 0, stream>>>(x2b2, W1_b + 1024 * 256, t_b1 + 1024, nullptr, mid_b, 1024, 1024);
-    gB_k<1024, 1><<<1, 256, 0, stream>>>(mid_b, W2_b + 256 * 1024, t_b2 + 256, h2, h2,
-                                         out_ln_g, out_ln_b, lstm_in_b, 512, c_out);
-
+    tail_k<1><<<1, 256, 0, stream>>>(ao2_b, Wo_b + 256 * 256, t_bo + 256,
+                                     h + (size_t)(S - 1) * BB * 256,
+                                     t_ln2_g + 256, t_ln2_b + 256,
+                                     W1_b + 1024 * 256, t_b1 + 1024,
+                                     W2_b + 256 * 1024, t_b2 + 256, nullptr,
+                                     out_ln_g, out_ln_b, lstm_in_b, 512, c_out);
     gL_k<0><<<16, 256, 0, stream>>>(lstm_in_b, Wc_b, cb2, cx, lstm_in_b, lstm_in_b + BB * 512,
                                     nullptr, nullptr, nullptr);
     gL_k<1><<<16, 256, 0, stream>>>(lstm_in_b + BB * 512, Wc_b + (size_t)1024 * 512, cb2 + 1024,
                                     cx + BB * DD, lstm_in_b + BB * 512, nullptr, c_out, cfinb, record_b);
-
-    head_k<<<(VV + 63) / 64, 256, 0, stream>>>(Wh, cfinb, head_b, out + (size_t)t * BB * VV);
-
     if (t < TT - 1) {
-      gA_k<0><<<dim3(17, 1), 256, 0, stream>>>(cfinb, Wrw_b, brw, rpwp, nullptr, 1036, 1036);
+      auxg_k<<<29, 256, 0, stream>>>(cfinb, Wrw_b, brw, rpwp, record_b, FR_b, brc, fp);
       if (t > 0)
-        passA_k<<<dim3(NN / 16, BB), 256, 0, stream>>>(memory, rpwp, dot_r, dot_w, norm2);
+        fusePA_k<<<786 + 8192, 256, 0, stream>>>(Wh, cfinb, head_b, out + (size_t)t * BB * VV,
+                                                 memory, rpwp, dot_r, dot_w, norm2);
+      else
+        fusePA_k<<<786, 256, 0, stream>>>(Wh, cfinb, head_b, out + (size_t)t * BB * VV,
+                                          memory, rpwp, dot_r, dot_w, norm2);
       addr_k<<<2 * BB, 256, 0, stream>>>(dot_r, dot_w, norm2, rpwp, read_w, write_w, ea, r_vec);
       if (t == 0)
         passB_k<1><<<dim3(NN / 128, BB), 256, 0, stream>>>(memory, write_w, read_w, ea, r_vec);
       else
         passB_k<0><<<dim3(NN / 128, BB), 256, 0, stream>>>(memory, write_w, read_w, ea, r_vec);
-    }
-  }
-}
+    } else {
+      fusePA_k<<<786, 256, 0, stream>>>(Wh, cfinb, head_b, out + (size_t)t * BB * VV,
+                                        memory, rpwp, dot_r, dot_w, norm2);
+    }
+  }
+}
```

Result: no change. 1.657 ms (-1.3%).
